# Performance work log

Measured on AMD Instinct MI355X. Metric: run time of the kernel, lower is better.

The kernel has to match this reference:

```python
import jax, jax.numpy as jnp
import numpy as np
import math

IN_FEATURES = 64
OUT_FEATURES = 64
GRID_SIZE = 17
GRID_RANGE = 2.5
BATCH = 8192


def setup_inputs() -> dict:
    key = jax.random.key(0)
    k1, k2, k3 = jax.random.split(key, 3)
    fan = 1.0 / math.sqrt(float(IN_FEATURES))
    inputs = jax.random.normal(k1, (BATCH, IN_FEATURES), dtype=jnp.float32)
    base_scale = jax.random.normal(k2, (IN_FEATURES, OUT_FEATURES), dtype=jnp.float32) * fan
    spline_weight = jax.random.normal(k3, (IN_FEATURES, OUT_FEATURES, GRID_SIZE), dtype=jnp.float32) * (0.1 * fan)
    output_bias = jnp.zeros((OUT_FEATURES,), dtype=jnp.float32)
    return {"inputs": inputs, "base_scale": base_scale, "spline_weight": spline_weight, "output_bias": output_bias}


def reference(inputs, base_scale, spline_weight, output_bias):
    # grid buffer: linspace over [-grid_range, grid_range]
    grid = jnp.linspace(-GRID_RANGE, GRID_RANGE, GRID_SIZE, dtype=jnp.float32)
    spacing = grid[1] - grid[0]
    # degree-1 B-spline (hat) basis: [B, in, grid]
    basis = jnp.maximum(1.0 - jnp.abs(inputs[..., None] - grid) / spacing, 0.0)
    # per-edge spline output: [B, in, out]
    spline_output = jnp.einsum('big,iog->bio', basis, spline_weight)
    # SiLU residual path, per edge
    base_output = jax.nn.silu(inputs)[..., None] * base_scale[None, :, :]
    edge_output = base_output + spline_output
    # sum incoming edges per destination node, normalized
    output = edge_output.sum(axis=1) / math.sqrt(float(IN_FEATURES)) + output_bias
    # dropout=0.0 -> identity
    return (output, edge_output, basis)
```

## Files before the change

### kernel.cpp

```cpp
#include <hip/hip_runtime.h>
#include <math.h>

#define NBATCH 8192
#define NIN 64
#define NOUT 64
#define NG 17

typedef float f32x4 __attribute__((ext_vector_type(4)));

#define OUT_ELEMS   (NBATCH * NOUT)
#define EDGE_ELEMS  (NBATCH * NIN * NOUT)
#define WT_FLOATS   (NIN * NG * NOUT)
#define WT_BYTES    (WT_FLOATS * sizeof(float))

__global__ void kan_transpose_w(const float* __restrict__ W, float* __restrict__ Wt) {
    int idx = blockIdx.x * blockDim.x + threadIdx.x;
    if (idx >= NIN * NOUT * NG) return;
    int i   = idx / (NOUT * NG);
    int rem = idx - i * (NOUT * NG);
    int o   = rem / NG;
    int g   = rem - o * NG;
    Wt[(i * NG + g) * NOUT + o] = W[idx];
}

__global__ __launch_bounds__(512) void kan_kernel(
    const float* __restrict__ x,
    const float* __restrict__ scale,
    const float* __restrict__ Wt,
    const float* __restrict__ bias,
    float* __restrict__ out,
    float* __restrict__ edge,
    float* __restrict__ basis)
{
    const int tid  = threadIdx.x;
    const int wave = tid >> 6;
    const int lane = tid & 63;
    const int b = blockIdx.x * 8 + wave;

    __shared__ float s_scale[NIN * NOUT];
    __shared__ f32x4 s_meta[8][64];

    {
        const f32x4* s4 = (const f32x4*)scale;
        f32x4* d4 = (f32x4*)s_scale;
        d4[tid]       = s4[tid];
        d4[tid + 512] = s4[tid + 512];
    }

    {
        float xv  = x[b * NIN + lane];
        float sig = 1.0f / (1.0f + __expf(-xv));
        float sl  = xv * sig;
        float u   = (xv + 2.5f) * 3.2f;
        float g0f = floorf(u);
        float t   = u - g0f;
        int   g0  = (int)g0f;
        float tw0 = ((unsigned)g0       < 17u) ? (1.0f - t) : 0.0f;
        float tw1 = ((unsigned)(g0 + 1) < 17u) ? t          : 0.0f;
        int g0c = min(max(g0, 0), 16);
        int g1c = min(max(g0 + 1, 0), 16);
        f32x4 m;
        m.x = sl; m.y = tw0; m.z = tw1;
        m.w = __uint_as_float((unsigned)g0c | ((unsigned)g1c << 16));
        s_meta[wave][lane] = m;
    }
    __syncthreads();

    {
        float* brow = basis + (size_t)b * (NIN * NG);
        #pragma unroll
        for (int k = 0; k < 4; ++k) {
            int p0 = (k * 64 + lane) * 4;
            f32x4 v;
            #pragma unroll
            for (int e = 0; e < 4; ++e) {
                int p = p0 + e;
                int i = (int)((unsigned)p / 17u);
                int g = p - i * 17;
                f32x4 m = s_meta[wave][i];
                unsigned gg = __float_as_uint(m.w);
                int g0c = (int)(gg & 0xffffu);
                int g1c = (int)(gg >> 16);
                v[e] = ((g == g0c) ? m.y : 0.0f) + ((g == g1c) ? m.z : 0.0f);
            }
            *(f32x4*)(brow + p0) = v;
        }
        if (lane < 16) {
            int p0 = (256 + lane) * 4;
            f32x4 v;
            #pragma unroll
            for (int e = 0; e < 4; ++e) {
                int p = p0 + e;
                int i = (int)((unsigned)p / 17u);
                int g = p - i * 17;
                f32x4 m = s_meta[wave][i];
                unsigned gg = __float_as_uint(m.w);
                int g0c = (int)(gg & 0xffffu);
                int g1c = (int)(gg >> 16);
                v[e] = ((g == g0c) ? m.y : 0.0f) + ((g == g1c) ? m.z : 0.0f);
            }
            *(f32x4*)(brow + p0) = v;
        }
    }

    f32x4 acc = {0.f, 0.f, 0.f, 0.f};
    float* erow = edge + (size_t)b * (NIN * NOUT);
    const int iq = lane >> 4;
    const int o  = (lane & 15) * 4;

    f32x4 m_n = s_meta[wave][iq];
    unsigned gg_n = __float_as_uint(m_n.w);
    f32x4 w0_n = *(const f32x4*)(Wt + (iq * NG + (int)(gg_n & 0xffffu)) * NOUT + o);
    f32x4 w1_n = *(const f32x4*)(Wt + (iq * NG + (int)(gg_n >> 16))     * NOUT + o);

    #pragma unroll
    for (int ib = 0; ib < NIN; ib += 4) {
        f32x4 m  = m_n;
        f32x4 w0 = w0_n;
        f32x4 w1 = w1_n;
        if (ib + 4 < NIN) {
            int i = ib + 4 + iq;
            m_n = s_meta[wave][i];
            unsigned gg = __float_as_uint(m_n.w);
            w0_n = *(const f32x4*)(Wt + (i * NG + (int)(gg & 0xffffu)) * NOUT + o);
            w1_n = *(const f32x4*)(Wt + (i * NG + (int)(gg >> 16))     * NOUT + o);
        }
        f32x4 sc = *(const f32x4*)(s_scale + (ib + iq) * NOUT + o);
        f32x4 v = m.x * sc + m.y * w0 + m.z * w1;
        *(f32x4*)(erow + ib * NOUT + lane * 4) = v;
        acc += v;
    }
    #pragma unroll
    for (int e = 0; e < 4; ++e) {
        float a = acc[e];
        a += __shfl_xor(a, 16);
        a += __shfl_xor(a, 32);
        acc[e] = a;
    }
    if (lane < 16) {
        f32x4 bi = *(const f32x4*)(bias + lane * 4);
        f32x4 r = acc * 0.125f + bi;
        *(f32x4*)(out + (size_t)b * NOUT + lane * 4) = r;
    }
}

extern "C" void kernel_launch(void* const* d_in, const int* in_sizes, int n_in,
                              void* d_out, int out_size, void* d_ws, size_t ws_size,
                              hipStream_t stream) {
    const float* x     = (const float*)d_in[0];
    const float* scale = (const float*)d_in[1];
    const float* W     = (const float*)d_in[2];
    const float* bias  = (const float*)d_in[3];

    float* out   = (float*)d_out;
    float* edge  = out + OUT_ELEMS;
    float* basis = edge + EDGE_ELEMS;

    float* Wt = (float*)d_ws;
    const int n = NIN * NOUT * NG;
    if (ws_size >= WT_BYTES) {
        kan_transpose_w<<<(n + 255) / 256, 256, 0, stream>>>(W, Wt);
        kan_kernel<<<dim3(NBATCH / 8), dim3(512), 0, stream>>>(x, scale, Wt, bias, out, edge, basis);
    }
}
```

Before: 38.07 us.

## Split basis writing into separate kernel and process two rows per wave

The fused kernel is split in two. One kernel writes the basis tensor, the other writes the edge and output tensors. Each wave now handles two batch rows in both kernels, so the per-block staging of base_scale into LDS is spread over more rows and the grids shrink. The cost is an extra kernel launch, a second read of the inputs, and no overlap between the two output streams inside one kernel.

```diff
diff --git a/kernel.cpp b/kernel.cpp
--- a/kernel.cpp
+++ b/kernel.cpp
@@ -23,19 +23,74 @@
     Wt[(i * NG + g) * NOUT + o] = W[idx];
 }
 
-__global__ __launch_bounds__(512) void kan_kernel(
+__device__ __forceinline__ f32x4 kan_meta(float xv) {
+    float sig = 1.0f / (1.0f + __expf(-xv));
+    float sl  = xv * sig;
+    float u   = (xv + 2.5f) * 3.2f;
+    float g0f = floorf(u);
+    float t   = u - g0f;
+    int   g0  = (int)g0f;
+    float tw0 = ((unsigned)g0       < 17u) ? (1.0f - t) : 0.0f;
+    float tw1 = ((unsigned)(g0 + 1) < 17u) ? t          : 0.0f;
+    int g0c = min(max(g0, 0), 16);
+    int g1c = min(max(g0 + 1, 0), 16);
+    f32x4 m;
+    m.x = sl; m.y = tw0; m.z = tw1;
+    m.w = __uint_as_float((unsigned)g0c | ((unsigned)g1c << 16));
+    return m;
+}
+
+#define BROWS 2
+__global__ __launch_bounds__(512) void kan_basis(
+    const float* __restrict__ x, float* __restrict__ basis)
+{
+    const int tid  = threadIdx.x;
+    const int wave = tid >> 6;
+    const int lane = tid & 63;
+    const int row0 = (blockIdx.x * 8 + wave) * BROWS;
+
+    __shared__ f32x4 s_meta[8][BROWS][64];
+    #pragma unroll
+    for (int r = 0; r < BROWS; ++r)
+        s_meta[wave][r][lane] = kan_meta(x[(row0 + r) * NIN + lane]);
+
+    float* bbase = basis + (size_t)row0 * (NIN * NG);
+    const int NF4 = BROWS * 272;
+    #pragma unroll
+    for (int k = 0; k < (NF4 + 63) / 64; ++k) {
+        int f4r = k * 64 + lane;
+        if (f4r < NF4) {
+            int row = (int)((unsigned)f4r / 272u);
+            int rem = f4r - row * 272;
+            f32x4 v;
+            #pragma unroll
+            for (int e = 0; e < 4; ++e) {
+                int p = rem * 4 + e;
+                int i = (int)((unsigned)p / 17u);
+                int g = p - i * 17;
+                f32x4 m = s_meta[wave][row][i];
+                unsigned gg = __float_as_uint(m.w);
+                v[e] = ((g == (int)(gg & 0xffffu)) ? m.y : 0.0f)
+                     + ((g == (int)(gg >> 16))     ? m.z : 0.0f);
+            }
+            *(f32x4*)(bbase + f4r * 4) = v;
+        }
+    }
+}
+
+#define EROWS 2
+__global__ __launch_bounds__(512) void kan_edge(
     const float* __restrict__ x,
     const float* __restrict__ scale,
     const float* __restrict__ Wt,
     const float* __restrict__ bias,
     float* __restrict__ out,
-    float* __restrict__ edge,
-    float* __restrict__ basis)
+    float* __restrict__ edge)
 {
     const int tid  = threadIdx.x;
     const int wave = tid >> 6;
     const int lane = tid & 63;
-    const int b = blockIdx.x * 8 + wave;
+    const int row0 = (blockIdx.x * 8 + wave) * EROWS;
 
     __shared__ float s_scale[NIN * NOUT];
     __shared__ f32x4 s_meta[8][64];
@@ -46,101 +101,56 @@
         d4[tid]       = s4[tid];
         d4[tid + 512] = s4[tid + 512];
     }
-
-    {
-        float xv  = x[b * NIN + lane];
-        float sig = 1.0f / (1.0f + __expf(-xv));
-        float sl  = xv * sig;
-        float u   = (xv + 2.5f) * 3.2f;
-        float g0f = floorf(u);
-        float t   = u - g0f;
-        int   g0  = (int)g0f;
-        float tw0 = ((unsigned)g0       < 17u) ? (1.0f - t) : 0.0f;
-        float tw1 = ((unsigned)(g0 + 1) < 17u) ? t          : 0.0f;
-        int g0c = min(max(g0, 0), 16);
-        int g1c = min(max(g0 + 1, 0), 16);
-        f32x4 m;
-        m.x = sl; m.y = tw0; m.z = tw1;
-        m.w = __uint_as_float((unsigned)g0c | ((unsigned)g1c << 16));
-        s_meta[wave][lane] = m;
-    }
     __syncthreads();
 
-    {
-        float* brow = basis + (size_t)b * (NIN * NG);
-        #pragma unroll
-        for (int k = 0; k < 4; ++k) {
-            int p0 = (k * 64 + lane) * 4;
-            f32x4 v;
-            #pragma unroll
-            for (int e = 0; e < 4; ++e) {
-                int p = p0 + e;
-                int i = (int)((unsigned)p / 17u);
-                int g = p - i * 17;
-                f32x4 m = s_meta[wave][i];
-                unsigned gg = __float_as_uint(m.w);
-                int g0c = (int)(gg & 0xffffu);
-                int g1c = (int)(gg >> 16);
-                v[e] = ((g == g0c) ? m.y : 0.0f) + ((g == g1c) ? m.z : 0.0f);
-            }
-            *(f32x4*)(brow + p0) = v;
-        }
-        if (lane < 16) {
-            int p0 = (256 + lane) * 4;
-            f32x4 v;
-            #pragma unroll
-            for (int e = 0; e < 4; ++e) {
-                int p = p0 + e;
-                int i = (int)((unsigned)p / 17u);
-                int g = p - i * 17;
-                f32x4 m = s_meta[wave][i];
-                unsigned gg = __float_as_uint(m.w);
-                int g0c = (int)(gg & 0xffffu);
-                int g1c = (int)(gg >> 16);
-                v[e] = ((g == g0c) ? m.y : 0.0f) + ((g == g1c) ? m.z : 0.0f);
-            }
-            *(f32x4*)(brow + p0) = v;
-        }
-    }
-
-    f32x4 acc = {0.f, 0.f, 0.f, 0.f};
-    float* erow = edge + (size_t)b * (NIN * NOUT);
     const int iq = lane >> 4;
     const int o  = (lane & 15) * 4;
-
-    f32x4 m_n = s_meta[wave][iq];
-    unsigned gg_n = __float_as_uint(m_n.w);
-    f32x4 w0_n = *(const f32x4*)(Wt + (iq * NG + (int)(gg_n & 0xffffu)) * NOUT + o);
-    f32x4 w1_n = *(const f32x4*)(Wt + (iq * NG + (int)(gg_n >> 16))     * NOUT + o);
+    f32x4 bi4 = *(const f32x4*)(bias + (lane & 15) * 4);
+    f32x4 outv[EROWS];
 
     #pragma unroll
-    for (int ib = 0; ib < NIN; ib += 4) {
-        f32x4 m  = m_n;
-        f32x4 w0 = w0_n;
-        f32x4 w1 = w1_n;
-        if (ib + 4 < NIN) {
-            int i = ib + 4 + iq;
-            m_n = s_meta[wave][i];
-            unsigned gg = __float_as_uint(m_n.w);
-            w0_n = *(const f32x4*)(Wt + (i * NG + (int)(gg & 0xffffu)) * NOUT + o);
-            w1_n = *(const f32x4*)(Wt + (i * NG + (int)(gg >> 16))     * NOUT + o);
+    for (int r = 0; r < EROWS; ++r) {
+        const int b = row0 + r;
+        s_meta[wave][lane] = kan_meta(x[b * NIN + lane]);
+
+        f32x4 acc = {0.f, 0.f, 0.f, 0.f};
+        float* erow = edge + (size_t)b * (NIN * NOUT);
+
+        f32x4 m_n = s_meta[wave][iq];
+        unsigned gg_n = __float_as_uint(m_n.w);
+        f32x4 w0_n = *(const f32x4*)(Wt + (iq * NG + (int)(gg_n & 0xffffu)) * NOUT + o);
+        f32x4 w1_n = *(const f32x4*)(Wt + (iq * NG + (int)(gg_n >> 16))     * NOUT + o);
+
+        #pragma unroll
+        for (int ib = 0; ib < NIN; ib += 4) {
+            f32x4 m  = m_n;
+            f32x4 w0 = w0_n;
+            f32x4 w1 = w1_n;
+            if (ib + 4 < NIN) {
+                int i = ib + 4 + iq;
+                m_n = s_meta[wave][i];
+                unsigned gg = __float_as_uint(m_n.w);
+                w0_n = *(const f32x4*)(Wt + (i * NG + (int)(gg & 0xffffu)) * NOUT + o);
+                w1_n = *(const f32x4*)(Wt + (i * NG + (int)(gg >> 16))     * NOUT + o);
+            }
+            f32x4 sc = *(const f32x4*)(s_scale + (ib + iq) * NOUT + o);
+            f32x4 v = m.x * sc + m.y * w0 + m.z * w1;
+            *(f32x4*)(erow + ib * NOUT + lane * 4) = v;
+            acc += v;
         }
-        f32x4 sc = *(const f32x4*)(s_scale + (ib + iq) * NOUT + o);
-        f32x4 v = m.x * sc + m.y * w0 + m.z * w1;
-        *(f32x4*)(erow + ib * NOUT + lane * 4) = v;
-        acc += v;
-    }
-    #pragma unroll
-    for (int e = 0; e < 4; ++e) {
-        float a = acc[e];
-        a += __shfl_xor(a, 16);
-        a += __shfl_xor(a, 32);
-        acc[e] = a;
+        #pragma unroll
+        for (int e = 0; e < 4; ++e) {
+            float a = acc[e];
+            a += __shfl_xor(a, 16);
+            a += __shfl_xor(a, 32);
+            acc[e] = a;
+        }
+        outv[r] = acc * 0.125f + bi4;
     }
     if (lane < 16) {
-        f32x4 bi = *(const f32x4*)(bias + lane * 4);
-        f32x4 r = acc * 0.125f + bi;
-        *(f32x4*)(out + (size_t)b * NOUT + lane * 4) = r;
+        #pragma unroll
+        for (int r = 0; r < EROWS; ++r)
+            *(f32x4*)(out + (size_t)(row0 + r) * NOUT + lane * 4) = outv[r];
     }
 }
 
@@ -160,6 +170,7 @@
     const int n = NIN * NOUT * NG;
     if (ws_size >= WT_BYTES) {
         kan_transpose_w<<<(n + 255) / 256, 256, 0, stream>>>(W, Wt);
-        kan_kernel<<<dim3(NBATCH / 8), dim3(512), 0, stream>>>(x, scale, Wt, bias, out, edge, basis);
+        kan_edge<<<dim3(NBATCH / (8 * EROWS)), dim3(512), 0, stream>>>(x, scale, Wt, bias, out, edge);
+        kan_basis<<<dim3(NBATCH / (8 * BROWS)), dim3(512), 0, stream>>>(x, basis);
     }
 }
```

Measured after the change: 40.12 us. +5.4%, slower.
